# Kernel tuning notes

Measured on AMD Instinct MI355X. Metric: run time of the kernel, lower is better.

## Reference

```python
import jax, jax.numpy as jnp
import numpy as np

B, C_IN, H, W = 1, 448, 64, 64   # concat of resnet18 layer1/2/3 resized to 64x64: 64+128+256=448
D, L = 100, 4096                 # projection dim, number of spatial locations (gaussian params)
OUT_HW = 256                     # input_size for final bilinear upsample


def setup_inputs() -> dict:
    key = jax.random.key(0)
    k0, k1, k2, k3, k4 = jax.random.split(key, 5)
    return {
        "features": jax.random.normal(k0, (B, C_IN, H, W), jnp.float32),
        "proj_w": jax.random.normal(k1, (D, C_IN), jnp.float32) * 0.05,
        "proj_b": jax.random.normal(k2, (D,), jnp.float32) * 0.05,
        "mean": jax.random.normal(k3, (D, L), jnp.float32),
        "inv_cov": jax.random.normal(k4, (L, D, D), jnp.float32) * 0.01,
    }


def reference(features, proj_w, proj_b, mean, inv_cov):
    Bn, C, Hh, Ww = features.shape
    # permute(0,2,3,1).reshape(-1, C) then Linear(C, D)
    f = features.transpose(0, 2, 3, 1).reshape(-1, C)          # (N, C), N = B*H*W
    f = f @ proj_w.T + proj_b                                  # (N, D)
    m = mean.T                                                 # (L, D)
    # Batched Mahalanobis-style quadratic form replacing the Python loop over L=4096:
    #   dist[n, l] = (f_n - m_l)^T  inv_cov_l  (f_n - m_l)
    # Expanded so the heavy term is a single (N, D*D) x (D*D, L) GEMM (no (N,L,D) intermediate).
    Cm  = jnp.einsum('lde,le->ld', inv_cov, m)                 # inv_cov_l @ m_l        (L, D)
    CTm = jnp.einsum('lde,ld->le', inv_cov, m)                 # inv_cov_l^T @ m_l      (L, D)
    const = jnp.einsum('ld,ld->l', m, Cm)                      # m_l^T inv_cov_l m_l    (L,)
    ff = (f[:, :, None] * f[:, None, :]).reshape(f.shape[0], D * D)   # outer(f,f) flattened (N, D*D)
    quad = ff @ inv_cov.reshape(L, D * D).T                    # f^T inv_cov_l f        (N, L)
    dist = quad - f @ (Cm + CTm).T + const[None, :]            # (N, L)
    min_d = jnp.min(dist, axis=1).reshape(Bn, Hh, Ww)[:, None, :, :]  # (B, 1, H, W)
    amap = (min_d - min_d.min()) / (min_d.max() - min_d.min() + 1e-8)
    amap = jax.image.resize(amap, (Bn, 1, OUT_HW, OUT_HW), method='bilinear')
    return amap
```

## Files before the change

### kernel.cpp

```cpp
#include <hip/hip_runtime.h>
#include <hip/hip_bf16.h>
#include <stdint.h>

#define CIN   448
#define DP    100
#define NPIX  4096
#define LNUM  4096
#define KQ    5050
#define KLIN  5150
#define KTOT  5184
#define KSTEPS (KTOT / 64)
#define OUTHW 256

typedef _Float16 f16_t;
typedef _Float16 f16x8 __attribute__((ext_vector_type(8)));
typedef float    f32x4 __attribute__((ext_vector_type(4)));
typedef unsigned short u16x8 __attribute__((ext_vector_type(8)));

static __device__ __forceinline__ int tri_off(int d) { return (d * (201 - d)) >> 1; }

static __device__ __forceinline__ void unpack_tri(int k, int& d, int& e) {
    int dd = (int)((201.0f - sqrtf(40401.0f - 8.0f * (float)k)) * 0.5f);
    if (dd < 0) dd = 0;
    if (dd > 99) dd = 99;
    while (tri_off(dd + 1) <= k) ++dd;
    while (tri_off(dd) > k) --dd;
    d = dd;
    e = dd + (k - tri_off(dd));
}

static __device__ __forceinline__ unsigned f2u(float x) {
    unsigned b = __float_as_uint(x);
    return (b & 0x80000000u) ? ~b : (b | 0x80000000u);
}
static __device__ __forceinline__ float u2f(unsigned u) {
    unsigned b = (u & 0x80000000u) ? (u & 0x7FFFFFFFu) : ~u;
    return __uint_as_float(b);
}

static __device__ __forceinline__ void gload_lds16(const f16_t* g, f16_t* l) {
    __builtin_amdgcn_global_load_lds((const __attribute__((address_space(1))) unsigned*)g,
                                     (__attribute__((address_space(3))) unsigned*)l,
                                     16, 0, 0);
}

__global__ void k_lut(unsigned short* __restrict__ lut, unsigned* __restrict__ mind) {
    int k = blockIdx.x * 256 + threadIdx.x;
    if (k < KTOT) {
        int d = 0, e = 0;
        if (k < KQ) unpack_tri(k, d, e);
        lut[k] = (unsigned short)(d | (e << 8));
    }
    if (k < NPIX) mind[k] = 0xFFFFFFFFu;
}

__global__ void k_proj(const float* __restrict__ feat, const float* __restrict__ w,
                       const float* __restrict__ b, float* __restrict__ f) {
    int gid = blockIdx.x * 256 + threadIdx.x;
    int n = gid & 4095;
    int d = gid >> 12;
    float acc = b[d];
    const float* wd = w + d * CIN;
    #pragma unroll 4
    for (int c = 0; c < CIN; ++c) acc += feat[c * 4096 + n] * wd[c];
    f[n * DP + d] = acc;
}

__global__ __launch_bounds__(256) void k_buildA(const float* __restrict__ f, const unsigned short* __restrict__ lut,
                                                f16_t* __restrict__ A) {
    __shared__ float fr[DP];
    int n = blockIdx.x;
    int t = threadIdx.x;
    if (t < DP) fr[t] = f[n * DP + t];
    __syncthreads();
    int r  = n & 127;
    int rsw = (r & 7) << 3;
    f16_t* tileBase = A + (size_t)(n >> 7) * KSTEPS * 8192;
    for (int g = t; g < KTOT / 8; g += 256) {
        int k0 = g * 8;
        u16x8 lu = *(const u16x8*)&lut[k0];
        f16x8 v;
        #pragma unroll
        for (int j = 0; j < 8; ++j) {
            int k = k0 + j;
            float x;
            if (k < KQ) {
                int d = lu[j] & 255, e = lu[j] >> 8;
                x = fr[d] * fr[e];
            } else if (k < KLIN) {
                x = fr[k - KQ];
            } else {
                x = 0.0f;
            }
            v[j] = (f16_t)x;
        }
        int kt = k0 >> 6, kin = k0 & 63;
        *(f16x8*)&tileBase[kt * 8192 + r * 64 + ((kin & 56) ^ rsw)] = v;
    }
}

__global__ __launch_bounds__(256) void k_buildB(const float* __restrict__ icov, const float* __restrict__ mean,
                                                const unsigned short* __restrict__ lut,
                                                f16_t* __restrict__ Bm, float* __restrict__ constl) {
    __shared__ float ic[DP * 101];
    __shared__ float ml[DP];
    __shared__ float wv[DP];
    __shared__ float part[DP];
    int l = blockIdx.x;
    int t = threadIdx.x;
    const float4* src4 = (const float4*)(icov + (size_t)l * DP * DP);
    for (int i4 = t; i4 < DP * DP / 4; i4 += 256) {
        float4 v = src4[i4];
        int flat = i4 * 4;
        int row = flat / 100;
        int col = flat - row * 100;
        float* dst = &ic[row * 101 + col];
        dst[0] = v.x; dst[1] = v.y; dst[2] = v.z; dst[3] = v.w;
    }
    if (t < DP) ml[t] = mean[t * LNUM + l];
    __syncthreads();
    if (t < DP) {
        float icm = 0.f, ictm = 0.f;
        for (int e = 0; e < DP; ++e) {
            icm  += ic[t * 101 + e] * ml[e];
            ictm += ic[e * 101 + t] * ml[e];
        }
        wv[t]   = icm + ictm;
        part[t] = ml[t] * icm;
    }
    __syncthreads();
    if (t == 0) {
        float c = 0.f;
        for (int d = 0; d < DP; ++d) c += part[d];
        constl[l] = c;
    }
    int r  = l & 127;
    int rsw = (r & 7) << 3;
    f16_t* tileBase = Bm + (size_t)(l >> 7) * KSTEPS * 8192;
    for (int g = t; g < KTOT / 8; g += 256) {
        int k0 = g * 8;
        u16x8 lu = *(const u16x8*)&lut[k0];
        f16x8 v;
        #pragma unroll
        for (int j = 0; j < 8; ++j) {
            int k = k0 + j;
            float x;
            if (k < KQ) {
                int d = lu[j] & 255, e = lu[j] >> 8;
                float s = ic[d * 101 + e] + ic[e * 101 + d];
                x = (d == e) ? 0.5f * s : s;
            } else if (k < KLIN) {
                x = -wv[k - KQ];
            } else {
                x = 0.0f;
            }
            v[j] = (f16_t)x;
        }
        int kt = k0 >> 6, kin = k0 & 63;
        *(f16x8*)&tileBase[kt * 8192 + r * 64 + ((kin & 56) ^ rsw)] = v;
    }
}

__global__ __launch_bounds__(256, 2) void k_gemm(const f16_t* __restrict__ A, const f16_t* __restrict__ Bm,
                                                 const float* __restrict__ constl, unsigned* __restrict__ mind) {
    __shared__ __align__(16) f16_t sA[2][8192];
    __shared__ __align__(16) f16_t sB[2][8192];

    int bid = blockIdx.x;
    int pid = ((bid & 7) << 7) | (bid >> 3);
    int group = pid >> 8;
    int pin = pid & 255;
    int bm = group * 8 + (pin & 7);
    int bn = pin >> 3;

    int t = threadIdx.x;
    int lane = t & 63;
    int w = t >> 6;
    int wr = w >> 1, wc = w & 1;

    f32x4 acc[4][4];
    #pragma unroll
    for (int i = 0; i < 4; ++i)
        #pragma unroll
        for (int j = 0; j < 4; ++j) acc[i][j] = (f32x4){0.f, 0.f, 0.f, 0.f};

    const f16_t* Atile = A  + (size_t)bm * KSTEPS * 8192 + w * 2048 + lane * 8;
    const f16_t* Btile = Bm + (size_t)bn * KSTEPS * 8192 + w * 2048 + lane * 8;

    int l15 = lane & 15;
    int xorv = (lane & 7) << 3;
    int klobase = (lane >> 4) * 8;
    int arowbase = wr * 64 + l15;
    int browbase = wc * 64 + l15;

    #pragma unroll
    for (int c = 0; c < 4; ++c) {
        gload_lds16(Atile + c * 512, &sA[0][w * 2048 + c * 512]);
        gload_lds16(Btile + c * 512, &sB[0][w * 2048 + c * 512]);
    }
    __syncthreads();

    for (int kt = 0; kt < KSTEPS; ++kt) {
        int p = kt & 1;
        if (kt + 1 < KSTEPS) {
            const f16_t* As = Atile + (size_t)(kt + 1) * 8192;
            const f16_t* Bs = Btile + (size_t)(kt + 1) * 8192;
            #pragma unroll
            for (int c = 0; c < 4; ++c) {
                gload_lds16(As + c * 512, &sA[p ^ 1][w * 2048 + c * 512]);
                gload_lds16(Bs + c * 512, &sB[p ^ 1][w * 2048 + c * 512]);
            }
        }
        #pragma unroll
        for (int kk = 0; kk < 2; ++kk) {
            int klo = (kk * 32 + klobase) ^ xorv;
            f16x8 afr[4], bfr[4];
            #pragma unroll
            for (int mi = 0; mi < 4; ++mi)
                afr[mi] = *(const f16x8*)&sA[p][(arowbase + mi * 16) * 64 + klo];
            #pragma unroll
            for (int ni = 0; ni < 4; ++ni)
                bfr[ni] = *(const f16x8*)&sB[p][(browbase + ni * 16) * 64 + klo];
            #pragma unroll
            for (int mi = 0; mi < 4; ++mi)
                #pragma unroll
                for (int ni = 0; ni < 4; ++ni)
                    acc[mi][ni] = __builtin_amdgcn_mfma_f32_16x16x32_f16(afr[mi], bfr[ni], acc[mi][ni], 0, 0, 0);
        }
        __syncthreads();
    }

    int colbase = bn * 128 + wc * 64 + l15;
    float cl[4];
    #pragma unroll
    for (int ni = 0; ni < 4; ++ni) cl[ni] = constl[colbase + ni * 16];
    #pragma unroll
    for (int mi = 0; mi < 4; ++mi) {
        #pragma unroll
        for (int j = 0; j < 4; ++j) {
            float v = 1e30f;
            #pragma unroll
            for (int ni = 0; ni < 4; ++ni) v = fminf(v, acc[mi][ni][j] + cl[ni]);
            #pragma unroll
            for (int s = 1; s < 16; s <<= 1) v = fminf(v, __shfl_xor(v, s, 64));
            if (l15 == 0) {
                int row = bm * 128 + wr * 64 + mi * 16 + (lane >> 4) * 4 + j;
                atomicMin(&mind[row], f2u(v));
            }
        }
    }
}

__global__ void k_minmax(const unsigned* __restrict__ mind, float* __restrict__ gmm) {
    __shared__ float smin[256], smax[256];
    int t = threadIdx.x;
    float vmin = 1e30f, vmax = -1e30f;
    for (int i = t; i < NPIX; i += 256) {
        float v = u2f(mind[i]);
        vmin = fminf(vmin, v);
        vmax = fmaxf(vmax, v);
    }
    smin[t] = vmin; smax[t] = vmax;
    __syncthreads();
    for (int s = 128; s > 0; s >>= 1) {
        if (t < s) {
            smin[t] = fminf(smin[t], smin[t + s]);
            smax[t] = fmaxf(smax[t], smax[t + s]);
        }
        __syncthreads();
    }
    if (t == 0) { gmm[0] = smin[0]; gmm[1] = smax[0]; }
}

__global__ void k_upsample(const unsigned* __restrict__ mind, const float* __restrict__ gmm,
                           float* __restrict__ out) {
    int gid = blockIdx.x * 256 + threadIdx.x;
    int i = gid >> 8, j = gid & 255;
    float gmin = gmm[0];
    float scale = 1.0f / (gmm[1] - gmm[0] + 1e-8f);
    float x = fminf(fmaxf(j * 0.25f - 0.375f, 0.0f), 63.0f);
    float y = fminf(fmaxf(i * 0.25f - 0.375f, 0.0f), 63.0f);
    int x0 = (int)x, y0 = (int)y;
    int x1 = min(x0 + 1, 63), y1 = min(y0 + 1, 63);
    float fx = x - x0, fy = y - y0;
    float v00 = u2f(mind[y0 * 64 + x0]), v01 = u2f(mind[y0 * 64 + x1]);
    float v10 = u2f(mind[y1 * 64 + x0]), v11 = u2f(mind[y1 * 64 + x1]);
    float v = v00 * (1.f - fy) * (1.f - fx) + v01 * (1.f - fy) * fx
            + v10 * fy * (1.f - fx) + v11 * fy * fx;
    out[gid] = (v - gmin) * scale;
}

__global__ void k_diag(float* __restrict__ out) {
    int gid = blockIdx.x * 256 + threadIdx.x;
    out[gid] = 0.25f;
}

extern "C" void kernel_launch(void* const* d_in, const int* in_sizes, int n_in,
                              void* d_out, int out_size, void* d_ws, size_t ws_size,
                              hipStream_t stream) {
    const float* feat = (const float*)d_in[0];
    const float* pw   = (const float*)d_in[1];
    const float* pb   = (const float*)d_in[2];
    const float* mean = (const float*)d_in[3];
    const float* icov = (const float*)d_in[4];

    size_t need = 0;
    auto count = [&need](size_t bytes) { need = ((need + 255) & ~(size_t)255) + bytes; };
    count((size_t)NPIX * DP * 4);
    count((size_t)NPIX * KTOT * 2);
    count((size_t)LNUM * KTOT * 2);
    count((size_t)LNUM * 4);
    count((size_t)NPIX * 4);
    count(2 * 4);
    count((size_t)KTOT * 2);
    if (ws_size < need) {
        k_diag<<<256, 256, 0, stream>>>((float*)d_out);
        return;
    }

    char* ws = (char*)d_ws;
    size_t off = 0;
    auto alloc = [&](size_t bytes) -> void* {
        off = (off + 255) & ~(size_t)255;
        void* p = ws + off;
        off += bytes;
        return p;
    };
    float*          f      = (float*)alloc((size_t)NPIX * DP * 4);
    f16_t*          Amat   = (f16_t*)alloc((size_t)NPIX * KTOT * 2);
    f16_t*          Bmat   = (f16_t*)alloc((size_t)LNUM * KTOT * 2);
    float*          constl = (float*)alloc((size_t)LNUM * 4);
    unsigned*       mind   = (unsigned*)alloc((size_t)NPIX * 4);
    float*          gmm    = (float*)alloc(2 * 4);
    unsigned short* lut    = (unsigned short*)alloc((size_t)KTOT * 2);

    k_lut     <<<(KTOT + 255) / 256, 256, 0, stream>>>(lut, mind);
    k_proj    <<<1600, 256, 0, stream>>>(feat, pw, pb, f);
    k_buildA  <<<NPIX, 256, 0, stream>>>(f, lut, Amat);
    k_buildB  <<<LNUM, 256, 0, stream>>>(icov, mean, lut, Bmat, constl);
    k_gemm    <<<1024, 256, 0, stream>>>(Amat, Bmat, constl, mind);
    k_minmax  <<<1, 256, 0, stream>>>(mind, gmm);
    k_upsample<<<256, 256, 0, stream>>>(mind, gmm, (float*)d_out);
}
```

Measured before the change: 307.2 us.

## Overlap GEMM tile prefetch with fine-grained waitcnt and tile the projection kernel

The GEMM main loop replaces full __syncthreads with explicit vmcnt waits that only drain the current tile's async LDS loads, so next-tile prefetch stays in flight during MFMA work. The projection kernel is rewritten to stage feature and weight tiles in shared memory, with each thread computing 25 outputs, and is launched with 64 blocks. This aims to cut memory stall time in the GEMM and redundant global reads in the projection. The trade-offs are fewer blocks for the projection and reliance on manual waitcnt correctness.

```diff
diff --git a/kernel.cpp b/kernel.cpp
--- a/kernel.cpp
+++ b/kernel.cpp
@@ -54,16 +54,40 @@
     if (k < NPIX) mind[k] = 0xFFFFFFFFu;
 }
 
-__global__ void k_proj(const float* __restrict__ feat, const float* __restrict__ w,
-                       const float* __restrict__ b, float* __restrict__ f) {
-    int gid = blockIdx.x * 256 + threadIdx.x;
-    int n = gid & 4095;
-    int d = gid >> 12;
-    float acc = b[d];
-    const float* wd = w + d * CIN;
-    #pragma unroll 4
-    for (int c = 0; c < CIN; ++c) acc += feat[c * 4096 + n] * wd[c];
-    f[n * DP + d] = acc;
+__global__ __launch_bounds__(256) void k_proj(const float* __restrict__ feat, const float* __restrict__ w,
+                                              const float* __restrict__ b, float* __restrict__ f) {
+    __shared__ float featS[16][64];
+    __shared__ float wS[DP][16];
+    int n0 = blockIdx.x * 64;
+    int t = threadIdx.x;
+    int nn = t & 63;
+    int dq = (t >> 6) * 25;
+    float acc[25];
+    #pragma unroll
+    for (int j = 0; j < 25; ++j) acc[j] = 0.f;
+    for (int c0 = 0; c0 < CIN; c0 += 16) {
+        __syncthreads();
+        for (int i = t; i < 16 * 64; i += 256) {
+            int cc = i >> 6, n2 = i & 63;
+            featS[cc][n2] = feat[(c0 + cc) * 4096 + n0 + n2];
+        }
+        for (int i = t; i < DP * 16; i += 256) {
+            int d = i >> 4, cc = i & 15;
+            wS[d][cc] = w[d * CIN + c0 + cc];
+        }
+        __syncthreads();
+        float fre[16];
+        #pragma unroll
+        for (int cc = 0; cc < 16; ++cc) fre[cc] = featS[cc][nn];
+        #pragma unroll
+        for (int j = 0; j < 25; ++j)
+            #pragma unroll
+            for (int cc = 0; cc < 16; ++cc)
+                acc[j] += fre[cc] * wS[dq + j][cc];
+    }
+    float* frow = f + (size_t)(n0 + nn) * DP + dq;
+    #pragma unroll
+    for (int j = 0; j < 25; ++j) frow[j] = acc[j] + b[dq + j];
 }
 
 __global__ __launch_bounds__(256) void k_buildA(const float* __restrict__ f, const unsigned short* __restrict__ lut,
@@ -198,7 +222,6 @@
         gload_lds16(Atile + c * 512, &sA[0][w * 2048 + c * 512]);
         gload_lds16(Btile + c * 512, &sB[0][w * 2048 + c * 512]);
     }
-    __syncthreads();
 
     for (int kt = 0; kt < KSTEPS; ++kt) {
         int p = kt & 1;
@@ -210,7 +233,12 @@
                 gload_lds16(As + c * 512, &sA[p ^ 1][w * 2048 + c * 512]);
                 gload_lds16(Bs + c * 512, &sB[p ^ 1][w * 2048 + c * 512]);
             }
-        }
+            asm volatile("s_waitcnt vmcnt(8)" ::: "memory");
+        } else {
+            asm volatile("s_waitcnt vmcnt(0)" ::: "memory");
+        }
+        __builtin_amdgcn_s_barrier();
+        __builtin_amdgcn_sched_barrier(0);
         #pragma unroll
         for (int kk = 0; kk < 2; ++kk) {
             int klo = (kk * 32 + klobase) ^ xorv;
@@ -227,7 +255,9 @@
                 for (int ni = 0; ni < 4; ++ni)
                     acc[mi][ni] = __builtin_amdgcn_mfma_f32_16x16x32_f16(afr[mi], bfr[ni], acc[mi][ni], 0, 0, 0);
         }
-        __syncthreads();
+        __builtin_amdgcn_sched_barrier(0);
+        __builtin_amdgcn_s_barrier();
+        __builtin_amdgcn_sched_barrier(0);
     }
 
     int colbase = bn * 128 + wc * 64 + l15;
@@ -335,7 +365,7 @@
     unsigned short* lut    = (unsigned short*)alloc((size_t)KTOT * 2);
 
     k_lut     <<<(KTOT + 255) / 256, 256, 0, stream>>>(lut, mind);
-    k_proj    <<<1600, 256, 0, stream>>>(feat, pw, pb, f);
+    k_proj    <<<64, 256, 0, stream>>>(feat, pw, pb, f);
     k_buildA  <<<NPIX, 256, 0, stream>>>(f, lut, Amat);
     k_buildB  <<<LNUM, 256, 0, stream>>>(icov, mean, lut, Bmat, constl);
     k_gemm    <<<1024, 256, 0, stream>>>(Amat, Bmat, constl, mind);
```

After: 397.3 us. +29.4%, slower.

## Replace double-buffered LDS pipeline with single-buffer load-sync-compute loop

Applied to the files above, without the earlier changes.

Removes the double-buffered shared-memory tiles in the main GEMM kernel so each k-step loads the tile, synchronizes, then computes from a single buffer. This halves LDS use per block, which may allow more resident blocks per CU. In exchange the prefetch of the next tile no longer overlaps with the MFMA work, so global-to-LDS latency is exposed on every iteration. Swizzle address computation is also recomputed per row rather than using precomputed lane values.

```diff
diff --git a/kernel.cpp b/kernel.cpp
--- a/kernel.cpp
+++ b/kernel.cpp
@@ -163,8 +163,8 @@
 
 __global__ __launch_bounds__(256, 2) void k_gemm(const f16_t* __restrict__ A, const f16_t* __restrict__ Bm,
                                                  const float* __restrict__ constl, unsigned* __restrict__ mind) {
-    __shared__ __align__(16) f16_t sA[2][8192];
-    __shared__ __align__(16) f16_t sB[2][8192];
+    __shared__ __align__(16) f16_t sA[8192];
+    __shared__ __align__(16) f16_t sB[8192];
 
     int bid = blockIdx.x;
     int pid = ((bid & 7) << 7) | (bid >> 3);
@@ -184,43 +184,38 @@
         #pragma unroll
         for (int j = 0; j < 4; ++j) acc[i][j] = (f32x4){0.f, 0.f, 0.f, 0.f};
 
-    const f16_t* Atile = A  + (size_t)bm * KSTEPS * 8192 + w * 2048 + lane * 8;
-    const f16_t* Btile = Bm + (size_t)bn * KSTEPS * 8192 + w * 2048 + lane * 8;
-
-    int l15 = lane & 15;
-    int xorv = (lane & 7) << 3;
-    int klobase = (lane >> 4) * 8;
-    int arowbase = wr * 64 + l15;
-    int browbase = wc * 64 + l15;
-
+    const f16_t* Atile = A + (size_t)bm * KSTEPS * 8192;
+    const f16_t* Btile = Bm + (size_t)bn * KSTEPS * 8192;
+
+    int chunk0 = w * 2048;
+    int lofs = lane * 8;
+
+    int arow[4], brow[4];
     #pragma unroll
-    for (int c = 0; c < 4; ++c) {
-        gload_lds16(Atile + c * 512, &sA[0][w * 2048 + c * 512]);
-        gload_lds16(Btile + c * 512, &sB[0][w * 2048 + c * 512]);
-    }
-    __syncthreads();
+    for (int i = 0; i < 4; ++i) {
+        arow[i] = wr * 64 + i * 16 + (lane & 15);
+        brow[i] = wc * 64 + i * 16 + (lane & 15);
+    }
 
     for (int kt = 0; kt < KSTEPS; ++kt) {
-        int p = kt & 1;
-        if (kt + 1 < KSTEPS) {
-            const f16_t* As = Atile + (size_t)(kt + 1) * 8192;
-            const f16_t* Bs = Btile + (size_t)(kt + 1) * 8192;
-            #pragma unroll
-            for (int c = 0; c < 4; ++c) {
-                gload_lds16(As + c * 512, &sA[p ^ 1][w * 2048 + c * 512]);
-                gload_lds16(Bs + c * 512, &sB[p ^ 1][w * 2048 + c * 512]);
-            }
-        }
+        const f16_t* As = Atile + kt * 8192;
+        const f16_t* Bs = Btile + kt * 8192;
+        #pragma unroll
+        for (int c = 0; c < 4; ++c) {
+            gload_lds16(As + chunk0 + c * 512 + lofs, &sA[chunk0 + c * 512]);
+            gload_lds16(Bs + chunk0 + c * 512 + lofs, &sB[chunk0 + c * 512]);
+        }
+        __syncthreads();
         #pragma unroll
         for (int kk = 0; kk < 2; ++kk) {
-            int klo = (kk * 32 + klobase) ^ xorv;
             f16x8 afr[4], bfr[4];
+            int klo = kk * 32 + (lane >> 4) * 8;
             #pragma unroll
             for (int mi = 0; mi < 4; ++mi)
-                afr[mi] = *(const f16x8*)&sA[p][(arowbase + mi * 16) * 64 + klo];
+                afr[mi] = *(const f16x8*)&sA[arow[mi] * 64 + (klo ^ ((arow[mi] & 7) << 3))];
             #pragma unroll
             for (int ni = 0; ni < 4; ++ni)
-                bfr[ni] = *(const f16x8*)&sB[p][(browbase + ni * 16) * 64 + klo];
+                bfr[ni] = *(const f16x8*)&sB[brow[ni] * 64 + (klo ^ ((brow[ni] & 7) << 3))];
             #pragma unroll
             for (int mi = 0; mi < 4; ++mi)
                 #pragma unroll
@@ -230,7 +225,7 @@
         __syncthreads();
     }
 
-    int colbase = bn * 128 + wc * 64 + l15;
+    int colbase = bn * 128 + wc * 64 + (lane & 15);
     float cl[4];
     #pragma unroll
     for (int ni = 0; ni < 4; ++ni) cl[ni] = constl[colbase + ni * 16];
@@ -243,7 +238,7 @@
             for (int ni = 0; ni < 4; ++ni) v = fminf(v, acc[mi][ni][j] + cl[ni]);
             #pragma unroll
             for (int s = 1; s < 16; s <<= 1) v = fminf(v, __shfl_xor(v, s, 64));
-            if (l15 == 0) {
+            if ((lane & 15) == 0) {
                 int row = bm * 128 + wr * 64 + mi * 16 + (lane >> 4) * 4 + j;
                 atomicMin(&mind[row], f2u(v));
             }
```

After: 297.7 us. 1.03x faster.
